# Optimization experiments

Hardware: AMD Instinct MI355X
Metric: run time of the kernel (lower is better)

## Reference

```python
import jax, jax.numpy as jnp
import numpy as np

C_S, C_Z, C_H, H, PQ, PV = 384, 128, 16, 12, 4, 8
B, N = 1, 512
W_C = (2.0 / (9.0 * PQ)) ** 0.5
W_L = (1.0 / 3.0) ** 0.5
OUT_IN = H * C_Z + H * C_H + H * PV * 3 + H * PV  # 2112


def setup_inputs() -> dict:
    key = jax.random.key(0)
    ks = jax.random.split(key, 16)
    s_i = jax.random.normal(ks[0], (B, N, C_S), jnp.float32)
    z_ij = jax.random.normal(ks[1], (B, N, N, C_Z), jnp.float32)
    # random rotation matrices via QR
    raw = jax.random.normal(ks[2], (B, N, 3, 3), jnp.float32)
    q, r = jnp.linalg.qr(raw)
    rots = q * jnp.sign(jnp.diagonal(r, axis1=-2, axis2=-1))[..., None, :]
    trans = jax.random.normal(ks[3], (B, N, 3), jnp.float32)
    sc = lambda fan_in: 1.0 / np.sqrt(fan_in)
    Wq = jax.random.normal(ks[4], (C_S, H * C_H), jnp.float32) * sc(C_S)
    Wk = jax.random.normal(ks[5], (C_S, H * C_H), jnp.float32) * sc(C_S)
    Wv = jax.random.normal(ks[6], (C_S, H * C_H), jnp.float32) * sc(C_S)
    Wqp = jax.random.normal(ks[7], (C_S, H * PQ * 3), jnp.float32) * sc(C_S)
    Wkp = jax.random.normal(ks[8], (C_S, H * PQ * 3), jnp.float32) * sc(C_S)
    Wvp = jax.random.normal(ks[9], (C_S, H * PV * 3), jnp.float32) * sc(C_S)
    Wb = jax.random.normal(ks[10], (C_Z, H), jnp.float32) * sc(C_Z)
    gamma = jax.random.normal(ks[11], (1, 1, 1, H), jnp.float32)
    Wout = jax.random.normal(ks[12], (OUT_IN, C_S), jnp.float32) * sc(OUT_IN)
    bout = jnp.zeros((C_S,), jnp.float32)
    return dict(s_i=s_i, z_ij=z_ij, rots=rots, trans=trans, Wq=Wq, Wk=Wk, Wv=Wv,
                Wqp=Wqp, Wkp=Wkp, Wvp=Wvp, Wb=Wb, gamma=gamma, Wout=Wout, bout=bout)


def reference(s_i, z_ij, rots, trans, Wq, Wk, Wv, Wqp, Wkp, Wvp, Wb, gamma, Wout, bout):
    b, n = s_i.shape[0], s_i.shape[1]
    q_h = (s_i @ Wq).reshape(b, n, H, C_H)
    k_h = (s_i @ Wk).reshape(b, n, H, C_H)
    v_h = (s_i @ Wv).reshape(b, n, H, C_H)
    q_hp = (s_i @ Wqp).reshape(b, n, H, PQ, 3)
    k_hp = (s_i @ Wkp).reshape(b, n, H, PQ, 3)
    v_hp = (s_i @ Wvp).reshape(b, n, H, PV, 3)
    b_ij = z_ij @ Wb  # (b,i,j,h)

    t = trans[:, :, None, None, :]  # (b,i,1,1,3)
    apply = lambda x: jnp.einsum('bixy,bihpy->bihpx', rots, x) + t
    inv_apply = lambda x: jnp.einsum('bixy,bihpx->bihpy', rots, x - t)

    qg = apply(q_hp)  # (b,i,h,p,3) global frame
    kg = apply(k_hp)
    # pairwise rigid point distance term: (b,i,j,h)
    diff = qg[:, :, None] - kg[:, None]  # (b,i,j,h,p,3)
    dist2 = jnp.sum(diff * diff, axis=(-1, -2))

    a_s = jnp.einsum('bihd,bjhd->bijh', q_h, k_h) / (C_H ** 0.5)
    a_rigid = (W_C / 2.0) * gamma * dist2
    a = jax.nn.softmax(W_L * (a_s + b_ij - a_rigid), axis=-2)  # softmax over j

    o_hat = jnp.einsum('bijh,bijd->bihd', a, z_ij)
    o = jnp.einsum('bijh,bjhd->bihd', a, v_h)
    vg = apply(v_hp)  # (b,j,h,p,3)
    o_hp = inv_apply(jnp.einsum('bijh,bjhpx->bihpx', a, vg))  # (b,i,h,pv,3)
    o_hp_norm = jnp.sqrt(jnp.sum(o_hp * o_hp, axis=-1))  # (b,i,h,pv)

    cat = jnp.concatenate([
        o_hat.reshape(b, n, H * C_Z),
        o.reshape(b, n, H * C_H),
        o_hp.reshape(b, n, H * PV * 3),
        o_hp_norm.reshape(b, n, H * PV),
    ], axis=-1)
    return cat @ Wout + bout
```

## Files before the change

kernel.cpp:

```cpp
#include <hip/hip_runtime.h>
#include <hip/hip_bf16.h>
#include <math.h>

#define NRES 512
#define CS   384
#define CZ   128
#define NH   12
#define PW   1152
#define JB   64
#define NCH  8
#define PSTRIDE32 1040
#define KS   6
#define KAW  352

static constexpr float WL_F      = 0.57735026918962576f;
static constexpr float HALF_WC_F = 0.11785113019775792f;

typedef __attribute__((ext_vector_type(8))) short short8v;
typedef __attribute__((ext_vector_type(4))) float floatx4;

__device__ __forceinline__ ushort f2b(float f) {
    union { float f; uint u; } v; v.f = f;
    return (ushort)((v.u + 0x7FFFu + ((v.u >> 16) & 1u)) >> 16);
}
__device__ __forceinline__ float b2f(ushort b) {
    union { uint u; float f; } v; v.u = ((uint)b) << 16; return v.f;
}

__global__ __launch_bounds__(256) void k_pack(
    const float* __restrict__ Wq, const float* __restrict__ Wk,
    const float* __restrict__ Wv, const float* __restrict__ Wqp,
    const float* __restrict__ Wkp, const float* __restrict__ Wvp,
    const float* __restrict__ Wb,
    float* __restrict__ Wcat, ushort* __restrict__ wbt16)
{
    const int c = blockIdx.x;
    for (int col = threadIdx.x; col < PW; col += 256) {
        float v;
        if (col < 192)      v = Wq [(size_t)c * 192 + col];
        else if (col < 384) v = Wk [(size_t)c * 192 + col - 192];
        else if (col < 576) v = Wv [(size_t)c * 192 + col - 384];
        else if (col < 720) v = Wqp[(size_t)c * 144 + col - 576];
        else if (col < 864) v = Wkp[(size_t)c * 144 + col - 720];
        else                v = Wvp[(size_t)c * 288 + col - 864];
        Wcat[(size_t)c * PW + col] = v;
    }
    if (blockIdx.x == 0) {
        for (int idx = threadIdx.x; idx < 16 * 128; idx += 256) {
            const int h = idx >> 7, cc = idx & 127;
            wbt16[idx] = (h < NH) ? f2b(WL_F * Wb[(size_t)cc * NH + h]) : (ushort)0;
        }
    }
}

__global__ __launch_bounds__(256) void k_wt(
    const float* __restrict__ Wout, ushort* __restrict__ woT)
{
    __shared__ ushort tile[64][72];
    const int k0 = blockIdx.x * 64, c0 = blockIdx.y * 64;
    for (int idx = threadIdx.x; idx < 4096; idx += 256) {
        const int r = idx >> 6, c = idx & 63;
        tile[r][c] = f2b(Wout[(size_t)(k0 + r) * 384 + c0 + c]);
    }
    __syncthreads();
    for (int idx = threadIdx.x; idx < 4096; idx += 256) {
        const int c = idx >> 6, r = idx & 63;
        woT[(size_t)(c0 + c) * 2112 + k0 + r] = tile[r][c];
    }
}

__global__ __launch_bounds__(256) void k_gemm(
    const float* __restrict__ s, const float* __restrict__ Wcat,
    const float* __restrict__ rots, const float* __restrict__ trans,
    float* __restrict__ P)
{
    const int tid = threadIdx.x;
    const int tx = tid & 15, ty = tid >> 4;
    const int n0 = blockIdx.x * 48;
    const int m0 = blockIdx.y * 32;
    __shared__ float As[32][34];
    __shared__ float Bs[32][50];
    __shared__ float rot_lds[32][12];

    if (n0 >= 576) {
        for (int idx = tid; idx < 32 * 12; idx += 256) {
            int r = idx / 12, q = idx % 12;
            rot_lds[r][q] = (q < 9) ? rots[(size_t)(m0 + r) * 9 + q]
                                    : trans[(size_t)(m0 + r) * 3 + q - 9];
        }
    }

    float acc[2][3];
    #pragma unroll
    for (int u = 0; u < 2; ++u)
        #pragma unroll
        for (int v = 0; v < 3; ++v) acc[u][v] = 0.f;

    for (int k0 = 0; k0 < CS; k0 += 32) {
        __syncthreads();
        #pragma unroll
        for (int l = 0; l < 4; ++l) {
            int idx = tid + l * 256;
            int kk = idx & 31, r = idx >> 5;
            As[kk][r] = s[(size_t)(m0 + r) * CS + k0 + kk];
        }
        #pragma unroll
        for (int l = 0; l < 6; ++l) {
            int idx = tid + l * 256;
            int kk = idx / 48, cc = idx % 48;
            Bs[kk][cc] = Wcat[(size_t)(k0 + kk) * PW + n0 + cc];
        }
        __syncthreads();
        #pragma unroll
        for (int kk = 0; kk < 32; ++kk) {
            const float2 a = *(const float2*)&As[kk][ty * 2];
            const float b0 = Bs[kk][tx * 3], b1 = Bs[kk][tx * 3 + 1], b2 = Bs[kk][tx * 3 + 2];
            acc[0][0] += a.x * b0; acc[0][1] += a.x * b1; acc[0][2] += a.x * b2;
            acc[1][0] += a.y * b0; acc[1][1] += a.y * b1; acc[1][2] += a.y * b2;
        }
    }

    #pragma unroll
    for (int u = 0; u < 2; ++u) {
        float v0 = acc[u][0], v1 = acc[u][1], v2 = acc[u][2];
        if (n0 >= 576) {
            const float* RT = rot_lds[ty * 2 + u];
            const float p0 = v0, p1 = v1, p2 = v2;
            v0 = RT[0] * p0 + RT[1] * p1 + RT[2] * p2 + RT[9];
            v1 = RT[3] * p0 + RT[4] * p1 + RT[5] * p2 + RT[10];
            v2 = RT[6] * p0 + RT[7] * p1 + RT[8] * p2 + RT[11];
        }
        float* dst = P + (size_t)(m0 + ty * 2 + u) * PW + n0 + tx * 3;
        dst[0] = v0; dst[1] = v1; dst[2] = v2;
    }
}

__global__ __launch_bounds__(128) void k_ka(
    const float* __restrict__ P, ushort* __restrict__ Kfull)
{
    const int j = blockIdx.x;
    const int tid = threadIdx.x;
    __shared__ float njs[NH];
    const float* kr  = P + (size_t)j * PW + 192;
    const float* kgr = P + (size_t)j * PW + 720;
    if (tid < NH) {
        float s = 0.f;
        #pragma unroll
        for (int e = 0; e < 12; ++e) { const float v = kgr[tid * 12 + e]; s += v * v; }
        njs[tid] = s;
    }
    __syncthreads();
    ushort* dst = Kfull + (size_t)j * KAW;
    for (int t = tid; t < KAW; t += 128) {
        float v;
        if (t < 192)       v = kr[t];
        else if (t < 336)  v = kgr[t - 192];
        else if (t < 348)  v = njs[t - 336];
        else if (t == 348) v = 1.0f;
        else               v = 0.f;
        dst[t] = f2b(v);
    }
}

__global__ __launch_bounds__(256) void k_flash(
    const float* __restrict__ z, const ushort* __restrict__ wbt16,
    const float* __restrict__ gamma, const float* __restrict__ P,
    const ushort* __restrict__ Kfull, uint* __restrict__ part)
{
    const int i   = blockIdx.x;
    const int jc  = blockIdx.y;
    const int j0  = jc * JB;
    const int tid = threadIdx.x;
    const int wid = tid >> 6, lane = tid & 63;

    __shared__ __align__(16) short zbT[128 * JB];
    __shared__ __align__(16) short BfT[16 * 488];
    __shared__ __align__(16) short ltb[16 * 64];
    __shared__ float ltf[16 * 68];
    __shared__ float pm[NH], ps[NH];

    uint* pb32   = part + ((size_t)i * NCH + jc) * PSTRIDE32;
    ushort* pb16 = (ushort*)pb32;
    float* pbf   = (float*)pb32;

    for (int idx = tid; idx < 16 * 488 / 2; idx += 256) ((uint*)BfT)[idx] = 0u;
    __syncthreads();

    {
        const float4* zr = (const float4*)(z + ((size_t)i * NRES + j0 + lane) * CZ + wid * 32);
        float f[32];
        #pragma unroll
        for (int k = 0; k < 8; ++k) {
            const float4 t = zr[k];
            f[k * 4 + 0] = t.x; f[k * 4 + 1] = t.y;
            f[k * 4 + 2] = t.z; f[k * 4 + 3] = t.w;
        }
        #pragma unroll
        for (int m = 0; m < 32; ++m) {
            const int c = wid * 32 + m;
            zbT[c * 64 + (((lane >> 3) ^ (c & 7)) * 8) + (lane & 7)] = (short)f2b(f[m]);
        }
    }
    {
        const float* prow = P + (size_t)i * PW;
        for (int t = tid; t < 360; t += 256) {
            if (t < 192) {
                const int h = t >> 4;
                BfT[h * 488 + t] = (short)f2b(0.25f * WL_F * prow[t]);
            } else if (t < 336) {
                const int e = t - 192, h = e / 12;
                BfT[h * 488 + t] =
                    (short)f2b(2.f * HALF_WC_F * WL_F * gamma[h] * prow[576 + e]);
            } else if (t < 348) {
                const int h = t - 336;
                BfT[h * 488 + t] = (short)f2b(-HALF_WC_F * WL_F * gamma[h]);
            } else {
                const int h = t - 348;
                float s = 0.f;
                #pragma unroll
                for (int e = 0; e < 12; ++e) {
                    const float v = prow[576 + h * 12 + e];
                    s += v * v;
                }
                BfT[h * 488 + 348] = (short)f2b(-HALF_WC_F * WL_F * gamma[h] * s);
            }
        }
        for (int idx = tid; idx < 1024; idx += 256) {
            const int h = idx >> 6, c2 = idx & 63;
            *(uint*)&BfT[h * 488 + 352 + c2 * 2] = ((const uint*)wbt16)[h * 64 + c2];
        }
    }
    __syncthreads();

    {
        const int jb = wid * 16 + (lane & 15);
        const int n  = lane & 15;
        const int ko = (lane >> 4) * 8;
        const ushort* arow = Kfull + (size_t)(j0 + jb) * KAW + ko;
        const short*  brow = &BfT[n * 488 + ko];
        const float*  za   = z + ((size_t)i * NRES + j0 + jb) * CZ + ko;
        floatx4 acc = {0.f, 0.f, 0.f, 0.f};
        #pragma unroll
        for (int st = 0; st < 11; ++st) {
            const short8v a = *(const short8v*)(arow + st * 32);
            const short8v b = *(const short8v*)(brow + st * 32);
            acc = __builtin_amdgcn_mfma_f32_16x16x32_bf16(a, b, acc, 0, 0, 0);
        }
        #pragma unroll
        for (int st = 0; st < 4; ++st) {
            const float4 f0 = *(const float4*)(za + st * 32);
            const float4 f1 = *(const float4*)(za + st * 32 + 4);
            short8v a;
            a[0] = (short)f2b(f0.x); a[1] = (short)f2b(f0.y);
            a[2] = (short)f2b(f0.z); a[3] = (short)f2b(f0.w);
            a[4] = (short)f2b(f1.x); a[5] = (short)f2b(f1.y);
            a[6] = (short)f2b(f1.z); a[7] = (short)f2b(f1.w);
            const short8v b = *(const short8v*)(brow + (11 + st) * 32);
            acc = __builtin_amdgcn_mfma_f32_16x16x32_bf16(a, b, acc, 0, 0, 0);
        }
        #pragma unroll
        for (int r = 0; r < 4; ++r)
            ltf[n * 68 + wid * 16 + (lane >> 4) * 4 + r] = acc[r];
    }
    __syncthreads();

    if (tid < 192) {
        const int h = tid >> 4, s = tid & 15;
        float4 v = *(const float4*)&ltf[h * 68 + s * 4];
        float m = fmaxf(fmaxf(v.x, v.y), fmaxf(v.z, v.w));
        #pragma unroll
        for (int o = 1; o < 16; o <<= 1) m = fmaxf(m, __shfl_xor(m, o));
        float4 e;
        e.x = __expf(v.x - m); e.y = __expf(v.y - m);
        e.z = __expf(v.z - m); e.w = __expf(v.w - m);
        float sum = e.x + e.y + e.z + e.w;
        #pragma unroll
        for (int o = 1; o < 16; o <<= 1) sum += __shfl_xor(sum, o);
        *(float4*)&ltf[h * 68 + s * 4] = e;
        const uint lo = (uint)f2b(e.x) | ((uint)f2b(e.y) << 16);
        const uint hi = (uint)f2b(e.z) | ((uint)f2b(e.w) << 16);
        uint* dst = (uint*)&ltb[h * 64 + (((s >> 1) ^ (h & 7)) * 8) + (s & 1) * 4];
        dst[0] = lo; dst[1] = hi;
        if (s == 0) { pm[h] = m; ps[h] = sum; }
    } else {
        const int tt = tid - 192;
        uint* dst = (uint*)&ltb[(12 + (tt >> 4)) * 64 + (tt & 15) * 4];
        dst[0] = 0u; dst[1] = 0u;
    }
    __syncthreads();

    {
        const int hrow = lane & 15;
        const int u0 = (lane >> 4), u1 = u0 + 4;
        const short8v a0 = *(const short8v*)&ltb[hrow * 64 + ((u0 ^ (hrow & 7)) * 8)];
        const short8v a1 = *(const short8v*)&ltb[hrow * 64 + ((u1 ^ (hrow & 7)) * 8)];
        #pragma unroll
        for (int t = 0; t < 2; ++t) {
            const int d = (wid * 2 + t) * 16 + (lane & 15);
            const short8v b0 = *(const short8v*)&zbT[d * 64 + ((u0 ^ (d & 7)) * 8)];
            const short8v b1 = *(const short8v*)&zbT[d * 64 + ((u1 ^ (d & 7)) * 8)];
            floatx4 acc = {0.f, 0.f, 0.f, 0.f};
            acc = __builtin_amdgcn_mfma_f32_16x16x32_bf16(a0, b0, acc, 0, 0, 0);
            acc = __builtin_amdgcn_mfma_f32_16x16x32_bf16(a1, b1, acc, 0, 0, 0);
            #pragma unroll
            for (int r = 0; r < 4; ++r) {
                const int h = u0 * 4 + r;
                if (h < NH) pb16[h * 128 + d] = f2b(acc[r]);
            }
        }
    }

    {
        float4* halfacc = (float4*)BfT;
        if (tid < 240) {
            const int half = tid / 120, col = tid % 120;
            int h;
            const float* base;
            if (col < 48) { h = col >> 2;               base = P + (size_t)j0 * PW + 384 + col * 4; }
            else          { const int cc = col - 48; h = cc / 6; base = P + (size_t)j0 * PW + 864 + cc * 4; }
            base += (size_t)(half * 32) * PW;
            const float* er = &ltf[h * 68 + half * 32];
            float ax = 0.f, ay = 0.f, az = 0.f, aw = 0.f;
            #pragma unroll 4
            for (int jj = 0; jj < 32; ++jj) {
                const float e = er[jj];
                const float4 v = *(const float4*)(base + (size_t)jj * PW);
                ax += e * v.x; ay += e * v.y; az += e * v.z; aw += e * v.w;
            }
            halfacc[tid] = make_float4(ax, ay, az, aw);
        }
        __syncthreads();
        if (tid < 120) {
            const float4 s0 = halfacc[tid], s1 = halfacc[tid + 120];
            const int off16 = (tid < 48) ? 1536 + tid * 4 : 1728 + (tid - 48) * 4;
            uint* dst = (uint*)&pb16[off16];
            dst[0] = (uint)f2b(s0.x + s1.x) | ((uint)f2b(s0.y + s1.y) << 16);
            dst[1] = (uint)f2b(s0.z + s1.z) | ((uint)f2b(s0.w + s1.w) << 16);
        }
        if (tid < NH) { pbf[1008 + tid] = pm[tid]; pbf[1020 + tid] = ps[tid]; }
    }
}

__global__ __launch_bounds__(256) void k_combine(
    const uint* __restrict__ part, const float* __restrict__ rots,
    const float* __restrict__ trans, ushort* __restrict__ cat16)
{
    const int i   = blockIdx.x;
    const int tid = threadIdx.x;
    __shared__ float wgt[NCH][NH];
    __shared__ float ohp[288];

    const uint* base = part + (size_t)i * NCH * PSTRIDE32;
    if (tid < NH) {
        const int h = tid;
        float mm[NCH];
        float M = -1e30f;
        #pragma unroll
        for (int c = 0; c < NCH; ++c) {
            mm[c] = ((const float*)(base + c * PSTRIDE32))[1008 + h];
            M = fmaxf(M, mm[c]);
        }
        float S = 0.f;
        #pragma unroll
        for (int c = 0; c < NCH; ++c) {
            const float w = __expf(mm[c] - M);
            S += w * ((const float*)(base + c * PSTRIDE32))[1020 + h];
            wgt[c][h] = w;
        }
        const float inv = 1.0f / S;
        #pragma unroll
        for (int c = 0; c < NCH; ++c) wgt[c][h] *= inv;
    }
    __syncthreads();

    ushort* crow = cat16 + (size_t)i * 2112;
    uint*   crowu = (uint*)crow;
    for (int idx2 = tid; idx2 < 768; idx2 += 256) {
        const int h = idx2 >> 6;
        float v0 = 0.f, v1 = 0.f;
        #pragma unroll
        for (int c = 0; c < NCH; ++c) {
            const uint u = base[c * PSTRIDE32 + idx2];
            const float w = wgt[c][h];
            v0 += b2f((ushort)u) * w;
            v1 += b2f((ushort)(u >> 16)) * w;
        }
        crowu[idx2] = (uint)f2b(v0) | ((uint)f2b(v1) << 16);
    }
    if (tid < 96) {
        const int h = tid >> 3;
        float v0 = 0.f, v1 = 0.f;
        #pragma unroll
        for (int c = 0; c < NCH; ++c) {
            const uint u = base[c * PSTRIDE32 + 768 + tid];
            const float w = wgt[c][h];
            v0 += b2f((ushort)u) * w;
            v1 += b2f((ushort)(u >> 16)) * w;
        }
        crowu[768 + tid] = (uint)f2b(v0) | ((uint)f2b(v1) << 16);
    }
    if (tid < 144) {
        const int h = tid / 12;
        float v0 = 0.f, v1 = 0.f;
        #pragma unroll
        for (int c = 0; c < NCH; ++c) {
            const uint u = base[c * PSTRIDE32 + 864 + tid];
            const float w = wgt[c][h];
            v0 += b2f((ushort)u) * w;
            v1 += b2f((ushort)(u >> 16)) * w;
        }
        ohp[tid * 2] = v0; ohp[tid * 2 + 1] = v1;
    }
    __syncthreads();

    if (tid < 96) {
        const int h = tid >> 3, p = tid & 7;
        float R[9];
        #pragma unroll
        for (int k = 0; k < 9; ++k) R[k] = rots[(size_t)i * 9 + k];
        const float g0 = ohp[h * 24 + p * 3 + 0] - trans[(size_t)i * 3 + 0];
        const float g1 = ohp[h * 24 + p * 3 + 1] - trans[(size_t)i * 3 + 1];
        const float g2 = ohp[h * 24 + p * 3 + 2] - trans[(size_t)i * 3 + 2];
        const float oy0 = R[0] * g0 + R[3] * g1 + R[6] * g2;
        const float oy1 = R[1] * g0 + R[4] * g1 + R[7] * g2;
        const float oy2 = R[2] * g0 + R[5] * g1 + R[8] * g2;
        crow[1728 + h * 24 + p * 3 + 0] = f2b(oy0);
        crow[1728 + h * 24 + p * 3 + 1] = f2b(oy1);
        crow[1728 + h * 24 + p * 3 + 2] = f2b(oy2);
        crow[2016 + h * 8 + p] = f2b(sqrtf(oy0 * oy0 + oy1 * oy1 + oy2 * oy2));
    }
}

__global__ __launch_bounds__(256) void k_out(
    const ushort* __restrict__ cat16, const ushort* __restrict__ woT,
    float* __restrict__ opart)
{
    const int tid = threadIdx.x;
    const int wid = tid >> 6, lane = tid & 63;
    const int wm = wid >> 1, wn = wid & 1;
    const int i0 = blockIdx.x * 32 + wm * 16;
    const int c0 = blockIdx.y * 32 + wn * 16;
    const int k0 = blockIdx.z * 352;
    const ushort* arow = cat16 + (size_t)(i0 + (lane & 15)) * 2112 + k0 + (lane >> 4) * 8;
    const ushort* brow = woT   + (size_t)(c0 + (lane & 15)) * 2112 + k0 + (lane >> 4) * 8;
    floatx4 acc = {0.f, 0.f, 0.f, 0.f};
    #pragma unroll
    for (int st = 0; st < 11; ++st) {
        const short8v a = *(const short8v*)(arow + st * 32);
        const short8v b = *(const short8v*)(brow + st * 32);
        acc = __builtin_amdgcn_mfma_f32_16x16x32_bf16(a, b, acc, 0, 0, 0);
    }
    float* ob = opart + (size_t)blockIdx.z * 512 * 384;
    #pragma unroll
    for (int r = 0; r < 4; ++r) {
        const int i = i0 + (lane >> 4) * 4 + r;
        ob[(size_t)i * 384 + c0 + (lane & 15)] = acc[r];
    }
}

__global__ __launch_bounds__(256) void k_outred(
    const float* __restrict__ opart, const float* __restrict__ bout,
    float* __restrict__ out)
{
    const int e4 = blockIdx.x * 256 + threadIdx.x;
    const float4* p = (const float4*)opart;
    const float4 b = ((const float4*)bout)[e4 % 96];
    float4 r = b;
    #pragma unroll
    for (int k = 0; k < KS; ++k) {
        const float4 v = p[e4 + k * 49152];
        r.x += v.x; r.y += v.y; r.z += v.z; r.w += v.w;
    }
    ((float4*)out)[e4] = r;
}

extern "C" void kernel_launch(void* const* d_in, const int* in_sizes, int n_in,
                              void* d_out, int out_size, void* d_ws, size_t ws_size,
                              hipStream_t stream)
{
    const float* s_i   = (const float*)d_in[0];
    const float* z_ij  = (const float*)d_in[1];
    const float* rots  = (const float*)d_in[2];
    const float* trans = (const float*)d_in[3];
    const float* Wq    = (const float*)d_in[4];
    const float* Wk    = (const float*)d_in[5];
    const float* Wv    = (const float*)d_in[6];
    const float* Wqp   = (const float*)d_in[7];
    const float* Wkp   = (const float*)d_in[8];
    const float* Wvp   = (const float*)d_in[9];
    const float* Wb    = (const float*)d_in[10];
    const float* gamma = (const float*)d_in[11];
    const float* Wout  = (const float*)d_in[12];
    const float* bout  = (const float*)d_in[13];
    float* ws = (float*)d_ws;
    float*  wcat  = ws;
    float*  P     = ws + 442368;
    uint*   part  = (uint*)(P + 589824);
    float*  opart = (float*)part;
    ushort* cat16 = (ushort*)(part + (size_t)512 * NCH * PSTRIDE32);
    ushort* wbt16 = cat16 + 1081344;
    ushort* kfull = wbt16 + 2048;
    ushort* woT   = kfull + 512 * KAW;
    float*  out   = (float*)d_out;

    hipLaunchKernelGGL(k_pack, dim3(384), dim3(256), 0, stream,
                       Wq, Wk, Wv, Wqp, Wkp, Wvp, Wb, wcat, wbt16);
    hipLaunchKernelGGL(k_wt, dim3(33, 6), dim3(256), 0, stream, Wout, woT);
    hipLaunchKernelGGL(k_gemm, dim3(24, 16), dim3(256), 0, stream,
                       s_i, wcat, rots, trans, P);
    hipLaunchKernelGGL(k_ka, dim3(512), dim3(128), 0, stream, P, kfull);
    hipLaunchKernelGGL(k_flash, dim3(512, NCH), dim3(256), 0, stream,
                       z_ij, wbt16, gamma, P, kfull, part);
    hipLaunchKernelGGL(k_combine, dim3(512), dim3(256), 0, stream,
                       part, rots, trans, cat16);
    hipLaunchKernelGGL(k_out, dim3(16, 12, KS), dim3(256), 0, stream,
                       cat16, woT, opart);
    hipLaunchKernelGGL(k_outred, dim3(192), dim3(256), 0, stream,
                       opart, bout, out);
}
```

Measured before the change: 137.6 us.

## Merge weight-prep kernels and shrink flash LDS footprint for higher occupancy

Fuses the weight pack and Wout transpose kernels into one launch to save a kernel launch. In the flash kernel, z is loaded once into registers and reused both as the bias-projection MFMA operand and for the transposed LDS copy, which removes a second global read of z. The Wb operand is now read directly from global memory. The BfT/ltf/ltb/halfacc buffers are aliased into one shared LDS region, and launch bounds request 6 blocks per SM to raise occupancy. This adds a sync and raises register pressure from holding the af fragments.

```diff
diff --git a/kernel.cpp b/kernel.cpp
--- a/kernel.cpp
+++ b/kernel.cpp
@@ -27,45 +27,46 @@
     union { uint u; float f; } v; v.u = ((uint)b) << 16; return v.f;
 }
 
-__global__ __launch_bounds__(256) void k_pack(
+__global__ __launch_bounds__(256) void k_prep(
     const float* __restrict__ Wq, const float* __restrict__ Wk,
     const float* __restrict__ Wv, const float* __restrict__ Wqp,
     const float* __restrict__ Wkp, const float* __restrict__ Wvp,
-    const float* __restrict__ Wb,
-    float* __restrict__ Wcat, ushort* __restrict__ wbt16)
-{
-    const int c = blockIdx.x;
-    for (int col = threadIdx.x; col < PW; col += 256) {
-        float v;
-        if (col < 192)      v = Wq [(size_t)c * 192 + col];
-        else if (col < 384) v = Wk [(size_t)c * 192 + col - 192];
-        else if (col < 576) v = Wv [(size_t)c * 192 + col - 384];
-        else if (col < 720) v = Wqp[(size_t)c * 144 + col - 576];
-        else if (col < 864) v = Wkp[(size_t)c * 144 + col - 720];
-        else                v = Wvp[(size_t)c * 288 + col - 864];
-        Wcat[(size_t)c * PW + col] = v;
-    }
-    if (blockIdx.x == 0) {
-        for (int idx = threadIdx.x; idx < 16 * 128; idx += 256) {
-            const int h = idx >> 7, cc = idx & 127;
-            wbt16[idx] = (h < NH) ? f2b(WL_F * Wb[(size_t)cc * NH + h]) : (ushort)0;
-        }
-    }
-}
-
-__global__ __launch_bounds__(256) void k_wt(
-    const float* __restrict__ Wout, ushort* __restrict__ woT)
+    const float* __restrict__ Wb, const float* __restrict__ Wout,
+    float* __restrict__ Wcat, ushort* __restrict__ wbt16,
+    ushort* __restrict__ woT)
 {
     __shared__ ushort tile[64][72];
-    const int k0 = blockIdx.x * 64, c0 = blockIdx.y * 64;
-    for (int idx = threadIdx.x; idx < 4096; idx += 256) {
-        const int r = idx >> 6, c = idx & 63;
-        tile[r][c] = f2b(Wout[(size_t)(k0 + r) * 384 + c0 + c]);
-    }
-    __syncthreads();
-    for (int idx = threadIdx.x; idx < 4096; idx += 256) {
-        const int c = idx >> 6, r = idx & 63;
-        woT[(size_t)(c0 + c) * 2112 + k0 + r] = tile[r][c];
+    const int bx = blockIdx.x;
+    if (bx < 384) {
+        const int c = bx;
+        for (int col = threadIdx.x; col < PW; col += 256) {
+            float v;
+            if (col < 192)      v = Wq [(size_t)c * 192 + col];
+            else if (col < 384) v = Wk [(size_t)c * 192 + col - 192];
+            else if (col < 576) v = Wv [(size_t)c * 192 + col - 384];
+            else if (col < 720) v = Wqp[(size_t)c * 144 + col - 576];
+            else if (col < 864) v = Wkp[(size_t)c * 144 + col - 720];
+            else                v = Wvp[(size_t)c * 288 + col - 864];
+            Wcat[(size_t)c * PW + col] = v;
+        }
+        if (bx == 0) {
+            for (int idx = threadIdx.x; idx < 16 * 128; idx += 256) {
+                const int h = idx >> 7, cc = idx & 127;
+                wbt16[idx] = (h < NH) ? f2b(WL_F * Wb[(size_t)cc * NH + h]) : (ushort)0;
+            }
+        }
+    } else {
+        const int t = bx - 384;
+        const int k0 = (t % 33) * 64, c0 = (t / 33) * 64;
+        for (int idx = threadIdx.x; idx < 4096; idx += 256) {
+            const int r = idx >> 6, c = idx & 63;
+            tile[r][c] = f2b(Wout[(size_t)(k0 + r) * 384 + c0 + c]);
+        }
+        __syncthreads();
+        for (int idx = threadIdx.x; idx < 4096; idx += 256) {
+            const int c = idx >> 6, r = idx & 63;
+            woT[(size_t)(c0 + c) * 2112 + k0 + r] = tile[r][c];
+        }
     }
 }
 
@@ -162,7 +163,7 @@
     }
 }
 
-__global__ __launch_bounds__(256) void k_flash(
+__global__ __launch_bounds__(256, 6) void k_flash(
     const float* __restrict__ z, const ushort* __restrict__ wbt16,
     const float* __restrict__ gamma, const float* __restrict__ P,
     const ushort* __restrict__ Kfull, uint* __restrict__ part)
@@ -174,93 +175,92 @@
     const int wid = tid >> 6, lane = tid & 63;
 
     __shared__ __align__(16) short zbT[128 * JB];
-    __shared__ __align__(16) short BfT[16 * 488];
-    __shared__ __align__(16) short ltb[16 * 64];
-    __shared__ float ltf[16 * 68];
+    __shared__ __align__(16) char  uni[10240];
     __shared__ float pm[NH], ps[NH];
+
+    short*  BfT     = (short*)uni;
+    float*  ltf     = (float*)uni;
+    short*  ltb     = (short*)(uni + 4352);
+    float4* halfacc = (float4*)(uni + 6400);
 
     uint* pb32   = part + ((size_t)i * NCH + jc) * PSTRIDE32;
     ushort* pb16 = (ushort*)pb32;
     float* pbf   = (float*)pb32;
 
-    for (int idx = tid; idx < 16 * 488 / 2; idx += 256) ((uint*)BfT)[idx] = 0u;
-    __syncthreads();
-
+    const int jb = wid * 16 + (lane & 15);
+    const int ko = (lane >> 4) * 8;
+
+    short8v af[4];
     {
-        const float4* zr = (const float4*)(z + ((size_t)i * NRES + j0 + lane) * CZ + wid * 32);
-        float f[32];
-        #pragma unroll
-        for (int k = 0; k < 8; ++k) {
-            const float4 t = zr[k];
-            f[k * 4 + 0] = t.x; f[k * 4 + 1] = t.y;
-            f[k * 4 + 2] = t.z; f[k * 4 + 3] = t.w;
-        }
-        #pragma unroll
-        for (int m = 0; m < 32; ++m) {
-            const int c = wid * 32 + m;
-            zbT[c * 64 + (((lane >> 3) ^ (c & 7)) * 8) + (lane & 7)] = (short)f2b(f[m]);
-        }
-    }
-    {
-        const float* prow = P + (size_t)i * PW;
-        for (int t = tid; t < 360; t += 256) {
-            if (t < 192) {
-                const int h = t >> 4;
-                BfT[h * 488 + t] = (short)f2b(0.25f * WL_F * prow[t]);
-            } else if (t < 336) {
-                const int e = t - 192, h = e / 12;
-                BfT[h * 488 + t] =
-                    (short)f2b(2.f * HALF_WC_F * WL_F * gamma[h] * prow[576 + e]);
-            } else if (t < 348) {
-                const int h = t - 336;
-                BfT[h * 488 + t] = (short)f2b(-HALF_WC_F * WL_F * gamma[h]);
-            } else {
-                const int h = t - 348;
-                float s = 0.f;
-                #pragma unroll
-                for (int e = 0; e < 12; ++e) {
-                    const float v = prow[576 + h * 12 + e];
-                    s += v * v;
-                }
-                BfT[h * 488 + 348] = (short)f2b(-HALF_WC_F * WL_F * gamma[h] * s);
-            }
-        }
-        for (int idx = tid; idx < 1024; idx += 256) {
-            const int h = idx >> 6, c2 = idx & 63;
-            *(uint*)&BfT[h * 488 + 352 + c2 * 2] = ((const uint*)wbt16)[h * 64 + c2];
-        }
-    }
-    __syncthreads();
-
-    {
-        const int jb = wid * 16 + (lane & 15);
-        const int n  = lane & 15;
-        const int ko = (lane >> 4) * 8;
-        const ushort* arow = Kfull + (size_t)(j0 + jb) * KAW + ko;
-        const short*  brow = &BfT[n * 488 + ko];
-        const float*  za   = z + ((size_t)i * NRES + j0 + jb) * CZ + ko;
-        floatx4 acc = {0.f, 0.f, 0.f, 0.f};
-        #pragma unroll
-        for (int st = 0; st < 11; ++st) {
-            const short8v a = *(const short8v*)(arow + st * 32);
-            const short8v b = *(const short8v*)(brow + st * 32);
-            acc = __builtin_amdgcn_mfma_f32_16x16x32_bf16(a, b, acc, 0, 0, 0);
-        }
-        #pragma unroll
-        for (int st = 0; st < 4; ++st) {
-            const float4 f0 = *(const float4*)(za + st * 32);
-            const float4 f1 = *(const float4*)(za + st * 32 + 4);
+        const float* za = z + ((size_t)i * NRES + j0 + jb) * CZ + ko;
+        #pragma unroll
+        for (int m = 0; m < 4; ++m) {
+            const float4 f0 = *(const float4*)(za + m * 32);
+            const float4 f1 = *(const float4*)(za + m * 32 + 4);
             short8v a;
             a[0] = (short)f2b(f0.x); a[1] = (short)f2b(f0.y);
             a[2] = (short)f2b(f0.z); a[3] = (short)f2b(f0.w);
             a[4] = (short)f2b(f1.x); a[5] = (short)f2b(f1.y);
             a[6] = (short)f2b(f1.z); a[7] = (short)f2b(f1.w);
-            const short8v b = *(const short8v*)(brow + (11 + st) * 32);
-            acc = __builtin_amdgcn_mfma_f32_16x16x32_bf16(a, b, acc, 0, 0, 0);
-        }
+            af[m] = a;
+            #pragma unroll
+            for (int e = 0; e < 8; ++e) {
+                const int c = ko + m * 32 + e;
+                zbT[c * 64 + (((jb >> 3) ^ (c & 7)) * 8) + (jb & 7)] = a[e];
+            }
+        }
+    }
+    {
+        const float* prow = P + (size_t)i * PW;
+        for (int t = tid; t < 12 * 352; t += 256) {
+            const int h = t / 352, k = t - h * 352;
+            float v = 0.f;
+            if (k < 192) {
+                if ((k >> 4) == h) v = 0.25f * WL_F * prow[k];
+            } else if (k < 336) {
+                const int e = k - 192;
+                if (e / 12 == h) v = 2.f * HALF_WC_F * WL_F * gamma[h] * prow[576 + e];
+            } else if (k < 348) {
+                if (k - 336 == h) v = -HALF_WC_F * WL_F * gamma[h];
+            } else if (k == 348) {
+                float ss = 0.f;
+                #pragma unroll
+                for (int e = 0; e < 12; ++e) {
+                    const float x = prow[576 + h * 12 + e];
+                    ss += x * x;
+                }
+                v = -HALF_WC_F * WL_F * gamma[h] * ss;
+            }
+            BfT[t] = (short)f2b(v);
+        }
+    }
+    __syncthreads();
+
+    floatx4 lacc = {0.f, 0.f, 0.f, 0.f};
+    {
+        const int n  = lane & 15;
+        const int nb = (n < NH) ? n : 0;
+        const ushort* arow = Kfull + (size_t)(j0 + jb) * KAW + ko;
+        const short*  brow = &BfT[nb * 352 + ko];
+        const ushort* wrow = wbt16 + n * 128 + ko;
+        #pragma unroll
+        for (int st = 0; st < 11; ++st) {
+            const short8v a = *(const short8v*)(arow + st * 32);
+            const short8v b = *(const short8v*)(brow + st * 32);
+            lacc = __builtin_amdgcn_mfma_f32_16x16x32_bf16(a, b, lacc, 0, 0, 0);
+        }
+        #pragma unroll
+        for (int st = 0; st < 4; ++st) {
+            const short8v b = *(const short8v*)(wrow + st * 32);
+            lacc = __builtin_amdgcn_mfma_f32_16x16x32_bf16(af[st], b, lacc, 0, 0, 0);
+        }
+    }
+    __syncthreads();
+    {
+        const int n = lane & 15;
         #pragma unroll
         for (int r = 0; r < 4; ++r)
-            ltf[n * 68 + wid * 16 + (lane >> 4) * 4 + r] = acc[r];
+            ltf[n * 68 + wid * 16 + (lane >> 4) * 4 + r] = lacc[r];
     }
     __syncthreads();
 
@@ -311,7 +311,6 @@
     }
 
     {
-        float4* halfacc = (float4*)BfT;
         if (tid < 240) {
             const int half = tid / 120, col = tid % 120;
             int h;
@@ -503,9 +502,8 @@
     ushort* woT   = kfull + 512 * KAW;
     float*  out   = (float*)d_out;
 
-    hipLaunchKernelGGL(k_pack, dim3(384), dim3(256), 0, stream,
-                       Wq, Wk, Wv, Wqp, Wkp, Wvp, Wb, wcat, wbt16);
-    hipLaunchKernelGGL(k_wt, dim3(33, 6), dim3(256), 0, stream, Wout, woT);
+    hipLaunchKernelGGL(k_prep, dim3(582), dim3(256), 0, stream,
+                       Wq, Wk, Wv, Wqp, Wkp, Wvp, Wb, Wout, wcat, wbt16, woT);
     hipLaunchKernelGGL(k_gemm, dim3(24, 16), dim3(256), 0, stream,
                        s_i, wcat, rots, trans, P);
     hipLaunchKernelGGL(k_ka, dim3(512), dim3(128), 0, stream, P, kfull);
```

Result: faster. 125.3 us (-8.9%).
